# Optimization experiments

Measured on AMD Instinct MI355X. Metric: run time of the kernel, lower is better.

Reference implementation:

```python
import jax, jax.numpy as jnp
import numpy as np

DIM = 1024
NUM_HEADS = 16
HEAD_DIM = DIM // NUM_HEADS
SCALE = HEAD_DIM ** -0.5


def setup_inputs() -> dict:
    key = jax.random.key(0)
    ks = jax.random.split(key, 13)
    B, Tq, Tk = 2, 1024, 4096
    s = DIM ** -0.5  # nn.Linear-like init scale
    inp = {
        'query': jax.random.normal(ks[0], (B, Tq, DIM), jnp.float32),
        'key': jax.random.normal(ks[1], (B, Tk, DIM), jnp.float32),
        'value': jax.random.normal(ks[2], (B, Tk, DIM), jnp.float32),
        'Wq': jax.random.normal(ks[3], (DIM, DIM), jnp.float32) * s,
        'bq': jnp.zeros((DIM,), jnp.float32),
        'Wk': jax.random.normal(ks[4], (DIM, DIM), jnp.float32) * s,
        'bk': jnp.zeros((DIM,), jnp.float32),
        'Wv': jax.random.normal(ks[5], (DIM, DIM), jnp.float32) * s,
        'bv': jnp.zeros((DIM,), jnp.float32),
        'Wo': jax.random.normal(ks[6], (DIM, DIM), jnp.float32) * s,
        'bo': jnp.zeros((DIM,), jnp.float32),
        'ln_gamma': jnp.ones((DIM,), jnp.float32),
        'ln_beta': jnp.zeros((DIM,), jnp.float32),
    }
    return inp


def _layer_norm(x, gamma, beta, eps=1e-5):
    mu = jnp.mean(x, axis=-1, keepdims=True)
    var = jnp.var(x, axis=-1, keepdims=True)
    return (x - mu) * jax.lax.rsqrt(var + eps) * gamma + beta


def reference(query, key, value, Wq, bq, Wk, bk, Wv, bv, Wo, bo, ln_gamma, ln_beta):
    B, Tq, D = query.shape
    Tk = key.shape[1]
    H, Hd = NUM_HEADS, HEAD_DIM
    # projections -> [B, H, T, Hd]
    q = (query @ Wq.T + bq).reshape(B, Tq, H, Hd).transpose(0, 2, 1, 3)
    k = (key @ Wk.T + bk).reshape(B, Tk, H, Hd).transpose(0, 2, 1, 3)
    v = (value @ Wv.T + bv).reshape(B, Tk, H, Hd).transpose(0, 2, 1, 3)
    scores = jnp.einsum('bhqd,bhkd->bhqk', q, k) * SCALE
    attn = jax.nn.softmax(scores, axis=-1)  # dropout is identity in eval
    out = jnp.einsum('bhqk,bhkd->bhqd', attn, v)
    out = out.transpose(0, 2, 1, 3).reshape(B, Tq, D)
    out = out @ Wo.T + bo
    out = _layer_norm(query + out, ln_gamma, ln_beta)
    return out, attn
```

## Files before the change

kernel.cpp:

```cpp
#include <hip/hip_runtime.h>
#include <hip/hip_bf16.h>

#define BATCH 2
#define TQ 1024
#define TK 4096
#define DIMSZ 1024
#define NH 16
#define HD 64
#define SCALE 0.125f

typedef __bf16 bf16x8 __attribute__((ext_vector_type(8)));
typedef float f32x4 __attribute__((ext_vector_type(4)));

static __device__ inline unsigned short f2bf(float x) {
  union { __bf16 h; unsigned short u; } v;
  v.h = (__bf16)x;
  return v.u;
}
static __device__ inline unsigned int pack2(float a, float b) {
  return (unsigned int)f2bf(a) | ((unsigned int)f2bf(b) << 16);
}

__global__ __launch_bounds__(256) void cast_all(
    const float* __restrict__ q, const float* __restrict__ k,
    const float* __restrict__ v, const float* __restrict__ wq,
    const float* __restrict__ wk, const float* __restrict__ wv,
    const float* __restrict__ wo, unsigned short* __restrict__ qo,
    unsigned short* __restrict__ ko, unsigned short* __restrict__ vo,
    unsigned short* __restrict__ wqo, unsigned short* __restrict__ wko,
    unsigned short* __restrict__ wvo, unsigned short* __restrict__ woo) {
  const float* src;
  unsigned short* dst;
  long n;
  switch (blockIdx.y) {
    case 0: src = q;  dst = qo;  n = (long)BATCH * TQ * DIMSZ; break;
    case 1: src = k;  dst = ko;  n = (long)BATCH * TK * DIMSZ; break;
    case 2: src = v;  dst = vo;  n = (long)BATCH * TK * DIMSZ; break;
    case 3: src = wq; dst = wqo; n = (long)DIMSZ * DIMSZ; break;
    case 4: src = wk; dst = wko; n = (long)DIMSZ * DIMSZ; break;
    case 5: src = wv; dst = wvo; n = (long)DIMSZ * DIMSZ; break;
    default: src = wo; dst = woo; n = (long)DIMSZ * DIMSZ; break;
  }
  const long stride = (long)gridDim.x * 256 * 8;
  for (long i = ((long)blockIdx.x * 256 + threadIdx.x) * 8; i < n; i += stride) {
    const float4 a = *(const float4*)&src[i];
    const float4 b = *(const float4*)&src[i + 4];
    uint4 o;
    o.x = pack2(a.x, a.y);
    o.y = pack2(a.z, a.w);
    o.z = pack2(b.x, b.y);
    o.w = pack2(b.z, b.w);
    *(uint4*)&dst[i] = o;
  }
}

template <bool OUT_BF16>
static __device__ __forceinline__ void gemm_body(
    const unsigned short* __restrict__ A, const unsigned short* __restrict__ B,
    const float* __restrict__ bias, void* __restrict__ Cout, int N, int K,
    int row0, int col0) {
  __shared__ unsigned short As[128][32];
  __shared__ unsigned short Bs[128][32];
  const int t = threadIdx.x;
  const int lane = t & 63, wv = t >> 6;
  const int wm = wv >> 1, wn = wv & 1;
  const int l15 = lane & 15, l4 = lane >> 4;

  f32x4 acc[4][4];
#pragma unroll
  for (int i = 0; i < 4; i++)
#pragma unroll
    for (int j = 0; j < 4; j++) acc[i][j] = (f32x4){0.f, 0.f, 0.f, 0.f};

  const int grow = lane >> 2;
  const int gcol = (lane & 3) * 8;
  const unsigned short* pA = &A[(size_t)(row0 + wv * 32 + grow) * K + gcol];
  const unsigned short* pB = &B[(size_t)(col0 + wv * 32 + grow) * K + gcol];

  for (int k0 = 0; k0 < K; k0 += 32) {
    __syncthreads();
#pragma unroll
    for (int c = 0; c < 2; c++) {
      __builtin_amdgcn_global_load_lds(
          (const __attribute__((address_space(1))) unsigned int*)(
              pA + (size_t)(c * 16) * K + k0),
          (__attribute__((address_space(3))) unsigned int*)&As[wv * 32 + c * 16][0],
          16, 0, 0);
      __builtin_amdgcn_global_load_lds(
          (const __attribute__((address_space(1))) unsigned int*)(
              pB + (size_t)(c * 16) * K + k0),
          (__attribute__((address_space(3))) unsigned int*)&Bs[wv * 32 + c * 16][0],
          16, 0, 0);
    }
    __syncthreads();
    bf16x8 av[4], bv[4];
#pragma unroll
    for (int f = 0; f < 4; f++) {
      av[f] = *(const bf16x8*)&As[wm * 64 + f * 16 + l15][l4 * 8];
      bv[f] = *(const bf16x8*)&Bs[wn * 64 + f * 16 + l15][l4 * 8];
    }
#pragma unroll
    for (int fm = 0; fm < 4; fm++)
#pragma unroll
      for (int fn = 0; fn < 4; fn++)
        acc[fm][fn] = __builtin_amdgcn_mfma_f32_16x16x32_bf16(
            av[fm], bv[fn], acc[fm][fn], 0, 0, 0);
  }

#pragma unroll
  for (int fm = 0; fm < 4; fm++) {
#pragma unroll
    for (int i = 0; i < 4; i++) {
      const int rr = row0 + wm * 64 + fm * 16 + l4 * 4 + i;
#pragma unroll
      for (int fn = 0; fn < 4; fn++) {
        const int c = col0 + wn * 64 + fn * 16 + l15;
        const float val = acc[fm][fn][i] + bias[c];
        if (OUT_BF16)
          ((unsigned short*)Cout)[(size_t)rr * N + c] = f2bf(val);
        else
          ((float*)Cout)[(size_t)rr * N + c] = val;
      }
    }
  }
}

__global__ __launch_bounds__(256) void proj_qkv(
    const unsigned short* __restrict__ qbf, const unsigned short* __restrict__ kbf,
    const unsigned short* __restrict__ vbf, const unsigned short* __restrict__ wqb,
    const unsigned short* __restrict__ wkb, const unsigned short* __restrict__ wvb,
    const float* __restrict__ bq, const float* __restrict__ bk,
    const float* __restrict__ bv, unsigned short* __restrict__ qb,
    unsigned short* __restrict__ kb, unsigned short* __restrict__ vbp) {
  const int y = blockIdx.y;
  const unsigned short *A, *B;
  const float* bias;
  unsigned short* C;
  int row0;
  if (y < 64) {
    A = kbf; B = wkb; bias = bk; C = kb; row0 = y * 128;
  } else if (y < 128) {
    A = vbf; B = wvb; bias = bv; C = vbp; row0 = (y - 64) * 128;
  } else {
    A = qbf; B = wqb; bias = bq; C = qb; row0 = (y - 128) * 128;
  }
  gemm_body<true>(A, B, bias, C, DIMSZ, DIMSZ, row0, blockIdx.x * 128);
}

__global__ __launch_bounds__(256) void proj_o(
    const unsigned short* __restrict__ A, const unsigned short* __restrict__ B,
    const float* __restrict__ bias, float* __restrict__ C) {
  gemm_body<false>(A, B, bias, C, DIMSZ, DIMSZ, blockIdx.y * 128,
                   blockIdx.x * 128);
}

__global__ __launch_bounds__(256) void transpose_v(
    const unsigned short* __restrict__ vb, unsigned short* __restrict__ vT) {
  const int z = blockIdx.z, b = z >> 4, h = z & 15;
  const int k0 = blockIdx.x * 64;
  __shared__ unsigned short Ts[64][68];
  const int t = threadIdx.x;
  const int c4 = (t & 15) * 4, r = t >> 4;
#pragma unroll
  for (int p = 0; p < 4; p++) {
    const int rr = r + p * 16;
    *(uint2*)&Ts[rr][c4] =
        *(const uint2*)&vb[(size_t)(b * TK + k0 + rr) * DIMSZ + h * HD + c4];
  }
  __syncthreads();
#pragma unroll
  for (int p = 0; p < 4; p++) {
    const int c2 = t + p * 256;
    const int d = c2 >> 4, k4 = (c2 & 15) * 4;
    uint2 o;
    o.x = (unsigned int)Ts[k4][d] | ((unsigned int)Ts[k4 + 1][d] << 16);
    o.y = (unsigned int)Ts[k4 + 2][d] | ((unsigned int)Ts[k4 + 3][d] << 16);
    *(uint2*)&vT[(size_t)(z * HD + d) * TK + k0 + k4] = o;
  }
}

__global__ __launch_bounds__(256) void attn_fused(
    const unsigned short* __restrict__ qb, const unsigned short* __restrict__ kb,
    const unsigned short* __restrict__ vT, float* __restrict__ attn,
    unsigned short* __restrict__ aout) {
  const int dsp = blockIdx.x;
  const int orig = (dsp & 7) * 64 + (dsp >> 3);
  const int z = orig >> 4, mb = orig & 15;
  const int b = z >> 4, h = z & 15;
  const int m0 = mb * 64;

  __shared__ unsigned short Qs[64][72];
  __shared__ unsigned short Ks[128][72];
  __shared__ unsigned short Vs[64][140];
  __shared__ unsigned short Ps[64][136];
  __shared__ float partial[64][2];
  __shared__ float rinv[64];

  const int t = threadIdx.x;
  const int lane = t & 63, wid = t >> 6;
  const int wm = wid >> 1, wn = wid & 1;
  const int l15 = lane & 15, l4 = lane >> 4;

#pragma unroll
  for (int p = 0; p < 2; p++) {
    const int idx = t + p * 256;
    const int r = idx >> 3, kc = idx & 7;
    *(uint4*)&Qs[r][kc * 8] =
        *(const uint4*)&qb[(size_t)(b * TQ + m0 + r) * DIMSZ + h * HD + kc * 8];
  }
  __syncthreads();
  bf16x8 aq[2][2];
#pragma unroll
  for (int fm = 0; fm < 2; fm++)
#pragma unroll
    for (int ks = 0; ks < 2; ks++)
      aq[fm][ks] = *(const bf16x8*)&Qs[wm * 32 + fm * 16 + l15][ks * 32 + l4 * 8];

  float rsum[8];
#pragma unroll
  for (int r = 0; r < 8; r++) rsum[r] = 0.f;

  for (int kt = 0; kt < TK / 128; kt++) {
    __syncthreads();
#pragma unroll
    for (int p = 0; p < 4; p++) {
      const int idx = t + p * 256;
      const int r = idx >> 3, kc = idx & 7;
      *(uint4*)&Ks[r][kc * 8] = *(const uint4*)&kb[
          (size_t)(b * TK + kt * 128 + r) * DIMSZ + h * HD + kc * 8];
    }
    __syncthreads();
    bf16x8 bk_[4][2];
#pragma unroll
    for (int fn = 0; fn < 4; fn++)
#pragma unroll
      for (int ks = 0; ks < 2; ks++)
        bk_[fn][ks] =
            *(const bf16x8*)&Ks[wn * 64 + fn * 16 + l15][ks * 32 + l4 * 8];
    f32x4 acc_s[2][4];
#pragma unroll
    for (int i = 0; i < 2; i++)
#pragma unroll
      for (int j = 0; j < 4; j++) acc_s[i][j] = (f32x4){0.f, 0.f, 0.f, 0.f};
#pragma unroll
    for (int ks = 0; ks < 2; ks++)
#pragma unroll
      for (int fm = 0; fm < 2; fm++)
#pragma unroll
        for (int fn = 0; fn < 4; fn++)
          acc_s[fm][fn] = __builtin_amdgcn_mfma_f32_16x16x32_bf16(
              aq[fm][ks], bk_[fn][ks], acc_s[fm][fn], 0, 0, 0);
#pragma unroll
    for (int fm = 0; fm < 2; fm++)
#pragma unroll
      for (int i = 0; i < 4; i++) {
        float s = 0.f;
#pragma unroll
        for (int fn = 0; fn < 4; fn++) s += __expf(acc_s[fm][fn][i] * SCALE);
        rsum[fm * 4 + i] += s;
      }
  }
#pragma unroll
  for (int off = 1; off < 16; off <<= 1)
#pragma unroll
    for (int r = 0; r < 8; r++) rsum[r] += __shfl_xor(rsum[r], off);
  if (l15 == 0) {
#pragma unroll
    for (int fm = 0; fm < 2; fm++)
#pragma unroll
      for (int i = 0; i < 4; i++)
        partial[wm * 32 + fm * 16 + l4 * 4 + i][wn] = rsum[fm * 4 + i];
  }
  __syncthreads();
  if (t < 64) rinv[t] = 1.f / (partial[t][0] + partial[t][1]);

  f32x4 acc_o[4];
#pragma unroll
  for (int j = 0; j < 4; j++) acc_o[j] = (f32x4){0.f, 0.f, 0.f, 0.f};

  float* attn_z = attn + (size_t)z * TQ * TK;

  for (int kt = 0; kt < TK / 128; kt++) {
    __syncthreads();
#pragma unroll
    for (int p = 0; p < 4; p++) {
      const int idx = t + p * 256;
      const int r = idx >> 3, kc = idx & 7;
      *(uint4*)&Ks[r][kc * 8] = *(const uint4*)&kb[
          (size_t)(b * TK + kt * 128 + r) * DIMSZ + h * HD + kc * 8];
    }
#pragma unroll
    for (int p = 0; p < 4; p++) {
      const int idx = t + p * 256;
      const int d = idx >> 4, kc = idx & 15;
      *(uint4*)&Vs[d][kc * 8] =
          *(const uint4*)&vT[(size_t)(z * HD + d) * TK + kt * 128 + kc * 8];
    }
    __syncthreads();

    bf16x8 bk_[4][2];
#pragma unroll
    for (int fn = 0; fn < 4; fn++)
#pragma unroll
      for (int ks = 0; ks < 2; ks++)
        bk_[fn][ks] =
            *(const bf16x8*)&Ks[wn * 64 + fn * 16 + l15][ks * 32 + l4 * 8];
    f32x4 acc_s[2][4];
#pragma unroll
    for (int i = 0; i < 2; i++)
#pragma unroll
      for (int j = 0; j < 4; j++) acc_s[i][j] = (f32x4){0.f, 0.f, 0.f, 0.f};
#pragma unroll
    for (int ks = 0; ks < 2; ks++)
#pragma unroll
      for (int fm = 0; fm < 2; fm++)
#pragma unroll
        for (int fn = 0; fn < 4; fn++)
          acc_s[fm][fn] = __builtin_amdgcn_mfma_f32_16x16x32_bf16(
              aq[fm][ks], bk_[fn][ks], acc_s[fm][fn], 0, 0, 0);

    float pv[2][4][4];
#pragma unroll
    for (int fm = 0; fm < 2; fm++)
#pragma unroll
      for (int i = 0; i < 4; i++) {
        const int row = wm * 32 + fm * 16 + l4 * 4 + i;
        const float iv = rinv[row];
#pragma unroll
        for (int fn = 0; fn < 4; fn++) {
          const int col = wn * 64 + fn * 16 + l15;
          const float p = __expf(acc_s[fm][fn][i] * SCALE) * iv;
          pv[fm][i][fn] = p;
          Ps[row][col] = f2bf(p);
        }
      }
    __syncthreads();

#pragma unroll
    for (int fm = 0; fm < 2; fm++)
#pragma unroll
      for (int i = 0; i < 4; i++) {
        const int row = wm * 32 + fm * 16 + l4 * 4 + i;
        float* arow = &attn_z[(size_t)(m0 + row) * TK + kt * 128];
#pragma unroll
        for (int fn = 0; fn < 4; fn++) {
          const int col = wn * 64 + fn * 16 + l15;
          __builtin_nontemporal_store(pv[fm][i][fn], &arow[col]);
        }
      }
#pragma unroll
    for (int ks2 = 0; ks2 < 4; ks2++) {
      const bf16x8 ap = *(const bf16x8*)&Ps[wid * 16 + l15][ks2 * 32 + l4 * 8];
#pragma unroll
      for (int fn = 0; fn < 4; fn++) {
        const bf16x8 bvv =
            *(const bf16x8*)&Vs[fn * 16 + l15][ks2 * 32 + l4 * 8];
        acc_o[fn] = __builtin_amdgcn_mfma_f32_16x16x32_bf16(ap, bvv,
                                                            acc_o[fn], 0, 0, 0);
      }
    }
  }

#pragma unroll
  for (int fn = 0; fn < 4; fn++)
#pragma unroll
    for (int i = 0; i < 4; i++) {
      const int rr = m0 + wid * 16 + l4 * 4 + i;
      aout[(size_t)(b * TQ + rr) * DIMSZ + h * HD + fn * 16 + l15] =
          f2bf(acc_o[fn][i]);
    }
}

__global__ __launch_bounds__(256) void residual_ln(
    const float* __restrict__ q, const float* __restrict__ y,
    const float* __restrict__ gamma, const float* __restrict__ beta,
    float* __restrict__ out) {
  __shared__ float w1[4];
  __shared__ float w2[4];
  const size_t base = (size_t)blockIdx.x * DIMSZ;
  const int t = threadIdx.x;

  float x[4];
  float s = 0.f;
#pragma unroll
  for (int i = 0; i < 4; i++) {
    const int c = t + i * 256;
    x[i] = q[base + c] + y[base + c];
    s += x[i];
  }
#pragma unroll
  for (int off = 32; off; off >>= 1) s += __shfl_xor(s, off);
  if ((t & 63) == 0) w1[t >> 6] = s;
  __syncthreads();
  const float mean = (w1[0] + w1[1] + w1[2] + w1[3]) * (1.f / DIMSZ);

  float vs = 0.f;
#pragma unroll
  for (int i = 0; i < 4; i++) {
    const float d = x[i] - mean;
    vs += d * d;
  }
#pragma unroll
  for (int off = 32; off; off >>= 1) vs += __shfl_xor(vs, off);
  if ((t & 63) == 0) w2[t >> 6] = vs;
  __syncthreads();
  const float var = (w2[0] + w2[1] + w2[2] + w2[3]) * (1.f / DIMSZ);
  const float rstd = rsqrtf(var + 1e-5f);

#pragma unroll
  for (int i = 0; i < 4; i++) {
    const int c = t + i * 256;
    out[base + c] = (x[i] - mean) * rstd * gamma[c] + beta[c];
  }
}

extern "C" void kernel_launch(void* const* d_in, const int* in_sizes, int n_in,
                              void* d_out, int out_size, void* d_ws,
                              size_t ws_size, hipStream_t stream) {
  const float* query = (const float*)d_in[0];
  const float* key   = (const float*)d_in[1];
  const float* value = (const float*)d_in[2];
  const float* Wq = (const float*)d_in[3];
  const float* bq = (const float*)d_in[4];
  const float* Wk = (const float*)d_in[5];
  const float* bk = (const float*)d_in[6];
  const float* Wv = (const float*)d_in[7];
  const float* bv = (const float*)d_in[8];
  const float* Wo = (const float*)d_in[9];
  const float* bo = (const float*)d_in[10];
  const float* ln_gamma = (const float*)d_in[11];
  const float* ln_beta  = (const float*)d_in[12];

  float* out  = (float*)d_out;
  float* attn = out + (size_t)BATCH * TQ * DIMSZ;

  const size_t MQ = (size_t)BATCH * TQ * DIMSZ;
  const size_t MK = (size_t)BATCH * TK * DIMSZ;
  const size_t MM = (size_t)DIMSZ * DIMSZ;

  unsigned short* ws = (unsigned short*)d_ws;
  unsigned short* qbf = ws;
  unsigned short* kbf = qbf + MQ;
  unsigned short* vbf = kbf + MK;
  unsigned short* wqb = vbf + MK;
  unsigned short* wkb = wqb + MM;
  unsigned short* wvb = wkb + MM;
  unsigned short* wob = wvb + MM;
  unsigned short* qb  = wob + MM;
  unsigned short* kb  = qb + MQ;
  unsigned short* vbp = kb + MK;
  unsigned short* vT = kbf;
  unsigned short* ab = qbf;
  float* ybuf = (float*)vbf;

  const dim3 blk(256);

  cast_all<<<dim3(1024, 7), blk, 0, stream>>>(query, key, value, Wq, Wk, Wv,
                                              Wo, qbf, kbf, vbf, wqb, wkb,
                                              wvb, wob);

  proj_qkv<<<dim3(DIMSZ / 128, 144), blk, 0, stream>>>(
      qbf, kbf, vbf, wqb, wkb, wvb, bq, bk, bv, qb, kb, vbp);

  transpose_v<<<dim3(TK / 64, 1, BATCH * NH), blk, 0, stream>>>(vbp, vT);

  attn_fused<<<dim3(512), blk, 0, stream>>>(qb, kb, vT, attn, ab);

  proj_o<<<dim3(DIMSZ / 128, (BATCH * TQ) / 128), blk, 0, stream>>>(ab, wob,
                                                                    bo, ybuf);

  residual_ln<<<dim3(BATCH * TQ), blk, 0, stream>>>(query, ybuf, ln_gamma,
                                                    ln_beta, out);
}
```

Measured before the change: 375.9 us.

## Fuse V transpose into QKV projection epilogue and interleave attn stores

The separate transpose_v kernel is removed. The V-projection blocks now stage their output through a shared-memory tile and write V directly in transposed [b,h,d,k] layout with 16-byte stores. This saves one kernel launch and a full read and write of the V intermediate. It also adds 16.5 KB of LDS to every proj_qkv block, which may lower occupancy. Separately, in attention the nontemporal stores of probabilities are now issued inline with the Ps writes, which shortens register live ranges.

```diff
diff --git a/kernel.cpp b/kernel.cpp
--- a/kernel.cpp
+++ b/kernel.cpp
@@ -54,13 +54,33 @@
   }
 }
 
-template <bool OUT_BF16>
-static __device__ __forceinline__ void gemm_body(
-    const unsigned short* __restrict__ A, const unsigned short* __restrict__ B,
-    const float* __restrict__ bias, void* __restrict__ Cout, int N, int K,
-    int row0, int col0) {
+__global__ __launch_bounds__(256) void proj_qkv(
+    const unsigned short* __restrict__ qbf, const unsigned short* __restrict__ kbf,
+    const unsigned short* __restrict__ vbf, const unsigned short* __restrict__ wqb,
+    const unsigned short* __restrict__ wkb, const unsigned short* __restrict__ wvb,
+    const float* __restrict__ bq, const float* __restrict__ bk,
+    const float* __restrict__ bv, unsigned short* __restrict__ qb,
+    unsigned short* __restrict__ kb, unsigned short* __restrict__ vT) {
   __shared__ unsigned short As[128][32];
   __shared__ unsigned short Bs[128][32];
+  __shared__ unsigned short T[64][132];
+
+  const int y = blockIdx.y;
+  const unsigned short *A, *B;
+  const float* bias;
+  int row0;
+  bool doT = false;
+  unsigned short* Cout;
+  if (y < 64) {
+    A = kbf; B = wkb; bias = bk; Cout = kb; row0 = y * 128;
+  } else if (y < 128) {
+    A = vbf; B = wvb; bias = bv; Cout = vT; row0 = (y - 64) * 128; doT = true;
+  } else {
+    A = qbf; B = wqb; bias = bq; Cout = qb; row0 = (y - 128) * 128;
+  }
+  const int col0 = blockIdx.x * 128;
+  const int K = DIMSZ, N = DIMSZ;
+
   const int t = threadIdx.x;
   const int lane = t & 63, wv = t >> 6;
   const int wm = wv >> 1, wn = wv & 1;
@@ -107,75 +127,116 @@
             av[fm], bv[fn], acc[fm][fn], 0, 0, 0);
   }
 
-#pragma unroll
-  for (int fm = 0; fm < 4; fm++) {
-#pragma unroll
-    for (int i = 0; i < 4; i++) {
-      const int rr = row0 + wm * 64 + fm * 16 + l4 * 4 + i;
-#pragma unroll
-      for (int fn = 0; fn < 4; fn++) {
-        const int c = col0 + wn * 64 + fn * 16 + l15;
-        const float val = acc[fm][fn][i] + bias[c];
-        if (OUT_BF16)
-          ((unsigned short*)Cout)[(size_t)rr * N + c] = f2bf(val);
-        else
-          ((float*)Cout)[(size_t)rr * N + c] = val;
-      }
-    }
-  }
-}
-
-__global__ __launch_bounds__(256) void proj_qkv(
-    const unsigned short* __restrict__ qbf, const unsigned short* __restrict__ kbf,
-    const unsigned short* __restrict__ vbf, const unsigned short* __restrict__ wqb,
-    const unsigned short* __restrict__ wkb, const unsigned short* __restrict__ wvb,
-    const float* __restrict__ bq, const float* __restrict__ bk,
-    const float* __restrict__ bv, unsigned short* __restrict__ qb,
-    unsigned short* __restrict__ kb, unsigned short* __restrict__ vbp) {
-  const int y = blockIdx.y;
-  const unsigned short *A, *B;
-  const float* bias;
-  unsigned short* C;
-  int row0;
-  if (y < 64) {
-    A = kbf; B = wkb; bias = bk; C = kb; row0 = y * 128;
-  } else if (y < 128) {
-    A = vbf; B = wvb; bias = bv; C = vbp; row0 = (y - 64) * 128;
+  if (!doT) {
+#pragma unroll
+    for (int fm = 0; fm < 4; fm++) {
+#pragma unroll
+      for (int i = 0; i < 4; i++) {
+        const int rr = row0 + wm * 64 + fm * 16 + l4 * 4 + i;
+#pragma unroll
+        for (int fn = 0; fn < 4; fn++) {
+          const int c = col0 + wn * 64 + fn * 16 + l15;
+          Cout[(size_t)rr * N + c] = f2bf(acc[fm][fn][i] + bias[c]);
+        }
+      }
+    }
   } else {
-    A = qbf; B = wqb; bias = bq; C = qb; row0 = (y - 128) * 128;
-  }
-  gemm_body<true>(A, B, bias, C, DIMSZ, DIMSZ, row0, blockIdx.x * 128);
+    const int bb = row0 >> 12;
+    const int krow0 = row0 & (TK - 1);
+#pragma unroll
+    for (int pass = 0; pass < 2; pass++) {
+      __syncthreads();
+      if (wn == pass) {
+#pragma unroll
+        for (int fm = 0; fm < 4; fm++)
+#pragma unroll
+          for (int fn = 0; fn < 4; fn++)
+#pragma unroll
+            for (int i = 0; i < 4; i++) {
+              const int cp = fn * 16 + l15;
+              const int row = wm * 64 + fm * 16 + l4 * 4 + i;
+              const int c = col0 + pass * 64 + cp;
+              T[cp][row] = f2bf(acc[fm][fn][i] + bias[c]);
+            }
+      }
+      __syncthreads();
+#pragma unroll
+      for (int qd = 0; qd < 4; qd++) {
+        const int idx = t + qd * 256;
+        const int cp = idx >> 4;
+        const int off8 = (idx & 15) * 8;
+        const uint4 v = *(const uint4*)&T[cp][off8];
+        *(uint4*)&vT[(size_t)(bb * 1024 + col0 + pass * 64 + cp) * TK +
+                     krow0 + off8] = v;
+      }
+    }
+  }
 }
 
 __global__ __launch_bounds__(256) void proj_o(
     const unsigned short* __restrict__ A, const unsigned short* __restrict__ B,
     const float* __restrict__ bias, float* __restrict__ C) {
-  gemm_body<false>(A, B, bias, C, DIMSZ, DIMSZ, blockIdx.y * 128,
-                   blockIdx.x * 128);
-}
-
-__global__ __launch_bounds__(256) void transpose_v(
-    const unsigned short* __restrict__ vb, unsigned short* __restrict__ vT) {
-  const int z = blockIdx.z, b = z >> 4, h = z & 15;
-  const int k0 = blockIdx.x * 64;
-  __shared__ unsigned short Ts[64][68];
+  __shared__ unsigned short As[128][32];
+  __shared__ unsigned short Bs[128][32];
+  const int row0 = blockIdx.y * 128, col0 = blockIdx.x * 128;
+  const int K = DIMSZ, N = DIMSZ;
   const int t = threadIdx.x;
-  const int c4 = (t & 15) * 4, r = t >> 4;
-#pragma unroll
-  for (int p = 0; p < 4; p++) {
-    const int rr = r + p * 16;
-    *(uint2*)&Ts[rr][c4] =
-        *(const uint2*)&vb[(size_t)(b * TK + k0 + rr) * DIMSZ + h * HD + c4];
-  }
-  __syncthreads();
-#pragma unroll
-  for (int p = 0; p < 4; p++) {
-    const int c2 = t + p * 256;
-    const int d = c2 >> 4, k4 = (c2 & 15) * 4;
-    uint2 o;
-    o.x = (unsigned int)Ts[k4][d] | ((unsigned int)Ts[k4 + 1][d] << 16);
-    o.y = (unsigned int)Ts[k4 + 2][d] | ((unsigned int)Ts[k4 + 3][d] << 16);
-    *(uint2*)&vT[(size_t)(z * HD + d) * TK + k0 + k4] = o;
+  const int lane = t & 63, wv = t >> 6;
+  const int wm = wv >> 1, wn = wv & 1;
+  const int l15 = lane & 15, l4 = lane >> 4;
+
+  f32x4 acc[4][4];
+#pragma unroll
+  for (int i = 0; i < 4; i++)
+#pragma unroll
+    for (int j = 0; j < 4; j++) acc[i][j] = (f32x4){0.f, 0.f, 0.f, 0.f};
+
+  const int grow = lane >> 2;
+  const int gcol = (lane & 3) * 8;
+  const unsigned short* pA = &A[(size_t)(row0 + wv * 32 + grow) * K + gcol];
+  const unsigned short* pB = &B[(size_t)(col0 + wv * 32 + grow) * K + gcol];
+
+  for (int k0 = 0; k0 < K; k0 += 32) {
+    __syncthreads();
+#pragma unroll
+    for (int c = 0; c < 2; c++) {
+      __builtin_amdgcn_global_load_lds(
+          (const __attribute__((address_space(1))) unsigned int*)(
+              pA + (size_t)(c * 16) * K + k0),
+          (__attribute__((address_space(3))) unsigned int*)&As[wv * 32 + c * 16][0],
+          16, 0, 0);
+      __builtin_amdgcn_global_load_lds(
+          (const __attribute__((address_space(1))) unsigned int*)(
+              pB + (size_t)(c * 16) * K + k0),
+          (__attribute__((address_space(3))) unsigned int*)&Bs[wv * 32 + c * 16][0],
+          16, 0, 0);
+    }
+    __syncthreads();
+    bf16x8 av[4], bv[4];
+#pragma unroll
+    for (int f = 0; f < 4; f++) {
+      av[f] = *(const bf16x8*)&As[wm * 64 + f * 16 + l15][l4 * 8];
+      bv[f] = *(const bf16x8*)&Bs[wn * 64 + f * 16 + l15][l4 * 8];
+    }
+#pragma unroll
+    for (int fm = 0; fm < 4; fm++)
+#pragma unroll
+      for (int fn = 0; fn < 4; fn++)
+        acc[fm][fn] = __builtin_amdgcn_mfma_f32_16x16x32_bf16(
+            av[fm], bv[fn], acc[fm][fn], 0, 0, 0);
+  }
+
+#pragma unroll
+  for (int fm = 0; fm < 4; fm++) {
+#pragma unroll
+    for (int i = 0; i < 4; i++) {
+      const int rr = row0 + wm * 64 + fm * 16 + l4 * 4 + i;
+#pragma unroll
+      for (int fn = 0; fn < 4; fn++) {
+        const int c = col0 + wn * 64 + fn * 16 + l15;
+        C[(size_t)rr * N + c] = acc[fm][fn][i] + bias[c];
+      }
+    }
   }
 }
 
@@ -319,35 +380,23 @@
           acc_s[fm][fn] = __builtin_amdgcn_mfma_f32_16x16x32_bf16(
               aq[fm][ks], bk_[fn][ks], acc_s[fm][fn], 0, 0, 0);
 
-    float pv[2][4][4];
 #pragma unroll
     for (int fm = 0; fm < 2; fm++)
 #pragma unroll
       for (int i = 0; i < 4; i++) {
         const int row = wm * 32 + fm * 16 + l4 * 4 + i;
         const float iv = rinv[row];
+        float* arow = &attn_z[(size_t)(m0 + row) * TK + kt * 128];
 #pragma unroll
         for (int fn = 0; fn < 4; fn++) {
           const int col = wn * 64 + fn * 16 + l15;
           const float p = __expf(acc_s[fm][fn][i] * SCALE) * iv;
-          pv[fm][i][fn] = p;
+          __builtin_nontemporal_store(p, &arow[col]);
           Ps[row][col] = f2bf(p);
         }
       }
     __syncthreads();
 
-#pragma unroll
-    for (int fm = 0; fm < 2; fm++)
-#pragma unroll
-      for (int i = 0; i < 4; i++) {
-        const int row = wm * 32 + fm * 16 + l4 * 4 + i;
-        float* arow = &attn_z[(size_t)(m0 + row) * TK + kt * 128];
-#pragma unroll
-        for (int fn = 0; fn < 4; fn++) {
-          const int col = wn * 64 + fn * 16 + l15;
-          __builtin_nontemporal_store(pv[fm][i][fn], &arow[col]);
-        }
-      }
 #pragma unroll
     for (int ks2 = 0; ks2 < 4; ks2++) {
       const bf16x8 ap = *(const bf16x8*)&Ps[wid * 16 + l15][ks2 * 32 + l4 * 8];
@@ -448,8 +497,7 @@
   unsigned short* wob = wvb + MM;
   unsigned short* qb  = wob + MM;
   unsigned short* kb  = qb + MQ;
-  unsigned short* vbp = kb + MK;
-  unsigned short* vT = kbf;
+  unsigned short* vT  = kb + MK;
   unsigned short* ab = qbf;
   float* ybuf = (float*)vbf;
 
@@ -460,9 +508,7 @@
                                               wvb, wob);
 
   proj_qkv<<<dim3(DIMSZ / 128, 144), blk, 0, stream>>>(
-      qbf, kbf, vbf, wqb, wkb, wvb, bq, bk, bv, qb, kb, vbp);
-
-  transpose_v<<<dim3(TK / 64, 1, BATCH * NH), blk, 0, stream>>>(vbp, vT);
+      qbf, kbf, vbf, wqb, wkb, wvb, bq, bk, bv, qb, kb, vT);
 
   attn_fused<<<dim3(512), blk, 0, stream>>>(qb, kb, vT, attn, ab);
 
```

After: 314.3 us. -16.4%, faster.
